# Performance work log

Measured on AMD Instinct MI355X. Metric: run time of the kernel, lower is better.

## Reference

```python
import jax, jax.numpy as jnp
import numpy as np

B, Cin, C, H, W = 2, 64, 128, 64, 64
D_INNER, N_STATE, DT_RANK, K = 256, 16, 8, 4


def _silu(x):
    return x * jax.nn.sigmoid(x)


def _layernorm(x, g, b, eps=1e-5):
    mu = x.mean(-1, keepdims=True)
    var = ((x - mu) ** 2).mean(-1, keepdims=True)
    return (x - mu) * jax.lax.rsqrt(var + eps) * g + b


def setup_inputs():
    key = jax.random.key(0)
    ks = jax.random.split(key, 16)
    f32 = jnp.float32
    inp = {}
    inp["x"] = jax.random.normal(ks[0], (B, Cin, H, W), f32)
    inp["convin_w"] = jax.random.normal(ks[1], (C, Cin), f32) * 0.05
    inp["convin_b"] = jnp.zeros((C,), f32)
    inp["ln_g"] = jnp.ones((C,), f32)
    inp["ln_b"] = jnp.zeros((C,), f32)
    inp["in_proj_w"] = jax.random.normal(ks[2], (2 * D_INNER, C), f32) * 0.05
    inp["conv_w"] = jax.random.normal(ks[3], (D_INNER, 1, 3, 3), f32) * 0.1
    inp["conv_b"] = jnp.zeros((D_INNER,), f32)
    inp["x_proj_w"] = jax.random.normal(ks[4], (K, DT_RANK + 2 * N_STATE, D_INNER), f32) * 0.05
    inp["dt_w"] = jax.random.normal(ks[5], (K, D_INNER, DT_RANK), f32) * 0.1
    inp["dt_b"] = jax.random.uniform(ks[6], (K, D_INNER), f32, -4.0, -1.0)
    inp["A_logs"] = jnp.log(jnp.tile(jnp.arange(1, N_STATE + 1, dtype=f32), (K, D_INNER, 1)))
    inp["Ds"] = jnp.ones((K, D_INNER), f32)
    inp["outnorm_g"] = jnp.ones((D_INNER,), f32)
    inp["outnorm_b"] = jnp.zeros((D_INNER,), f32)
    inp["out_proj_w"] = jax.random.normal(ks[7], (C, D_INNER), f32) * 0.05
    inp["ca_fc1_w"] = jax.random.normal(ks[8], (C // 16, C), f32) * 0.1
    inp["ca_fc2_w"] = jax.random.normal(ks[9], (C, C // 16), f32) * 0.1
    inp["gn_g"] = jnp.ones((C,), f32)
    inp["gn_b"] = jnp.zeros((C,), f32)
    return inp


def _selective_scan(u, delta, A, Bm, Cm, Ds):
    # u, delta: (B,K,d,L); A: (K,d,N); Bm, Cm: (B,K,N,L); Ds: (K,d)
    def step(h, inp):
        u_t, dt, B_t, C_t = inp
        dA = jnp.exp(dt[..., None] * A)                      # (B,K,d,N)
        h = h * dA + dt[..., None] * B_t[:, :, None, :] * u_t[..., None]
        y = jnp.einsum('bkdn,bkn->bkd', h, C_t)
        return h, y
    step = jax.checkpoint(step)
    seq = (jnp.moveaxis(u, -1, 0), jnp.moveaxis(delta, -1, 0),
           jnp.moveaxis(Bm, -1, 0), jnp.moveaxis(Cm, -1, 0))
    h0 = jnp.zeros(u.shape[:3] + (A.shape[-1],), u.dtype)
    _, ys = jax.lax.scan(step, h0, seq)                      # (L,B,K,d)
    y = jnp.moveaxis(ys, 0, -1)                              # (B,K,d,L)
    return y + u * Ds[None, :, :, None]


def reference(x, convin_w, convin_b, ln_g, ln_b, in_proj_w, conv_w, conv_b,
              x_proj_w, dt_w, dt_b, A_logs, Ds, outnorm_g, outnorm_b,
              out_proj_w, ca_fc1_w, ca_fc2_w, gn_g, gn_b):
    L = H * W
    # 1x1 conv in
    x1 = jnp.einsum('bchw,oc->bohw', x, convin_w) + convin_b[None, :, None, None]
    m = x1.transpose(0, 2, 3, 1)                             # (B,H,W,C)
    # VSSBlock: LN -> SS2D -> residual
    m_ln = _layernorm(m, ln_g, ln_b)
    xz = m_ln @ in_proj_w.T                                  # (B,H,W,2*d_inner)
    xm, z = jnp.split(xz, 2, axis=-1)
    xm = xm.transpose(0, 3, 1, 2)                            # (B,d,H,W)
    xm = jax.lax.conv_general_dilated(xm, conv_w, (1, 1), [(1, 1), (1, 1)],
                                      feature_group_count=D_INNER)
    xm = _silu(xm + conv_b[None, :, None, None])
    x_flat = xm.reshape(B, D_INNER, L)
    x_tr = xm.transpose(0, 1, 3, 2).reshape(B, D_INNER, L)
    xs = jnp.stack([x_flat, x_tr, jnp.flip(x_flat, -1), jnp.flip(x_tr, -1)], axis=1)
    x_dbl = jnp.einsum('bkdl,kcd->bkcl', xs, x_proj_w)
    dts, Bs, Cs = jnp.split(x_dbl, [DT_RANK, DT_RANK + N_STATE], axis=2)
    delta = jax.nn.softplus(jnp.einsum('bkrl,kdr->bkdl', dts, dt_w) + dt_b[None, :, :, None])
    A = -jnp.exp(A_logs)                                     # (K,d,N)
    out_y = _selective_scan(xs, delta, A, Bs, Cs, Ds)        # (B,4,d,L)
    y0 = out_y[:, 0]
    y1 = out_y[:, 1].reshape(B, D_INNER, W, H).transpose(0, 1, 3, 2).reshape(B, D_INNER, L)
    y2 = jnp.flip(out_y[:, 2], -1)
    y3 = jnp.flip(out_y[:, 3], -1).reshape(B, D_INNER, W, H).transpose(0, 1, 3, 2).reshape(B, D_INNER, L)
    y = (y0 + y1 + y2 + y3).transpose(0, 2, 1).reshape(B, H, W, D_INNER)
    y = _layernorm(y, outnorm_g, outnorm_b)
    y = y * _silu(z)
    m_out = m + y @ out_proj_w.T                             # (B,H,W,C)
    mamba = m_out.transpose(0, 3, 1, 2)                      # (B,C,H,W)
    # CBAM-style channel attention
    def mlp(v):
        return jax.nn.relu(v @ ca_fc1_w.T) @ ca_fc2_w.T
    avg = mamba.mean((2, 3))
    mx = mamba.max((2, 3))
    att = jax.nn.sigmoid(mlp(avg) + mlp(mx))[:, :, None, None]
    ca = mamba * att
    # GroupNorm(2 groups) + SiLU + residual
    g = ca.reshape(B, 2, -1)
    mu = g.mean(-1, keepdims=True)
    var = ((g - mu) ** 2).mean(-1, keepdims=True)
    g = ((g - mu) * jax.lax.rsqrt(var + 1e-5)).reshape(B, C, H, W)
    g = g * gn_g[None, :, None, None] + gn_b[None, :, None, None]
    return _silu(g) + x1
```

## Files before the change

### kernel.cpp

```cpp
#include <hip/hip_runtime.h>
#include <math.h>


#define DEV __device__ __forceinline__

typedef __attribute__((ext_vector_type(8))) short bf16x8;
typedef __attribute__((ext_vector_type(4))) float f32x4;

DEV float sigm_(float x){ return 1.f/(1.f+__expf(-x)); }
DEV float silu_(float x){ return x*sigm_(x); }
DEV float sp_(float x){ return (x>15.f)? x : __logf(1.f+__expf(x)); }

DEV unsigned short f2bf(float f){
  union{float f; unsigned u;} v; v.f=f;
  unsigned r=v.u + 0x7FFFu + ((v.u>>16)&1u);
  return (unsigned short)(r>>16);
}
DEV float bf2f(unsigned short h){ union{unsigned u; float f;} v; v.u=((unsigned)h)<<16; return v.f; }

DEV int pos_dir(int k, int l){
  switch(k&3){
    case 0: return l;
    case 1: return ((l&63)<<6)|(l>>6);
    case 2: return 4095-l;
    default:{ int m=4095-l; return ((m&63)<<6)|(m>>6); }
  }
}

DEV bf16x8 cvt_frag(const float* p){
  float4 q0=*(const float4*)p, q1=*(const float4*)(p+4);
  bf16x8 t;
  t[0]=(short)f2bf(q0.x); t[1]=(short)f2bf(q0.y); t[2]=(short)f2bf(q0.z); t[3]=(short)f2bf(q0.w);
  t[4]=(short)f2bf(q1.x); t[5]=(short)f2bf(q1.y); t[6]=(short)f2bf(q1.z); t[7]=(short)f2bf(q1.w);
  return t;
}

__global__ __launch_bounds__(256) void k_x1ln(const float* __restrict__ x,
    const float* __restrict__ W, const float* __restrict__ bias,
    const float* __restrict__ g, const float* __restrict__ be,
    float* __restrict__ x1, unsigned short* __restrict__ mlnb){
  const int b=blockIdx.y, p0=blockIdx.x*64;
  __shared__ float sw[64*132];
  __shared__ float sx[64*68];
  __shared__ float red[2][16][68];
  __shared__ float smu[64], srs[64];
  const int tid=threadIdx.x, tx=tid&15, ty=tid>>4;
  for (int i=tid;i<8192;i+=256){ int c=i&63,o=i>>6; sw[c*132+o]=W[o*64+c]; }
  for (int i=tid;i<4096;i+=256){ int c=i>>6,p=i&63; sx[c*68+p]=x[((size_t)(b*64+c))*4096+p0+p]; }
  __syncthreads();
  float acc[8][4]={};
  for (int c=0;c<64;++c){
    float4 a0=*(const float4*)&sw[c*132+ty*8];
    float4 a1=*(const float4*)&sw[c*132+ty*8+4];
    float4 bv=*(const float4*)&sx[c*68+tx*4];
    acc[0][0]=fmaf(a0.x,bv.x,acc[0][0]); acc[0][1]=fmaf(a0.x,bv.y,acc[0][1]); acc[0][2]=fmaf(a0.x,bv.z,acc[0][2]); acc[0][3]=fmaf(a0.x,bv.w,acc[0][3]);
    acc[1][0]=fmaf(a0.y,bv.x,acc[1][0]); acc[1][1]=fmaf(a0.y,bv.y,acc[1][1]); acc[1][2]=fmaf(a0.y,bv.z,acc[1][2]); acc[1][3]=fmaf(a0.y,bv.w,acc[1][3]);
    acc[2][0]=fmaf(a0.z,bv.x,acc[2][0]); acc[2][1]=fmaf(a0.z,bv.y,acc[2][1]); acc[2][2]=fmaf(a0.z,bv.z,acc[2][2]); acc[2][3]=fmaf(a0.z,bv.w,acc[2][3]);
    acc[3][0]=fmaf(a0.w,bv.x,acc[3][0]); acc[3][1]=fmaf(a0.w,bv.y,acc[3][1]); acc[3][2]=fmaf(a0.w,bv.z,acc[3][2]); acc[3][3]=fmaf(a0.w,bv.w,acc[3][3]);
    acc[4][0]=fmaf(a1.x,bv.x,acc[4][0]); acc[4][1]=fmaf(a1.x,bv.y,acc[4][1]); acc[4][2]=fmaf(a1.x,bv.z,acc[4][2]); acc[4][3]=fmaf(a1.x,bv.w,acc[4][3]);
    acc[5][0]=fmaf(a1.y,bv.x,acc[5][0]); acc[5][1]=fmaf(a1.y,bv.y,acc[5][1]); acc[5][2]=fmaf(a1.y,bv.z,acc[5][2]); acc[5][3]=fmaf(a1.y,bv.w,acc[5][3]);
    acc[6][0]=fmaf(a1.z,bv.x,acc[6][0]); acc[6][1]=fmaf(a1.z,bv.y,acc[6][1]); acc[6][2]=fmaf(a1.z,bv.z,acc[6][2]); acc[6][3]=fmaf(a1.z,bv.w,acc[6][3]);
    acc[7][0]=fmaf(a1.w,bv.x,acc[7][0]); acc[7][1]=fmaf(a1.w,bv.y,acc[7][1]); acc[7][2]=fmaf(a1.w,bv.z,acc[7][2]); acc[7][3]=fmaf(a1.w,bv.w,acc[7][3]);
  }
  float xr[8][4];
  #pragma unroll
  for (int i=0;i<8;++i){
    float bs=bias[ty*8+i];
    #pragma unroll
    for (int j=0;j<4;++j) xr[i][j]=acc[i][j]+bs;
  }
  {
    float s[4]={},s2[4]={};
    #pragma unroll
    for (int i=0;i<8;++i)
      #pragma unroll
      for (int j=0;j<4;++j){ s[j]+=xr[i][j]; s2[j]=fmaf(xr[i][j],xr[i][j],s2[j]); }
    #pragma unroll
    for (int j=0;j<4;++j){ red[0][ty][tx*4+j]=s[j]; red[1][ty][tx*4+j]=s2[j]; }
  }
  __syncthreads();
  if (tid<64){
    float S=0.f,S2=0.f;
    #pragma unroll
    for (int t=0;t<16;++t){ S+=red[0][t][tid]; S2+=red[1][t][tid]; }
    float mu=S*(1.f/128.f), var=S2*(1.f/128.f)-mu*mu;
    smu[tid]=mu; srs[tid]=rsqrtf(var+1e-5f);
  }
  __syncthreads();
  float* lnt=sw;
  #pragma unroll
  for (int i=0;i<8;++i){
    int o=ty*8+i;
    float gv=g[o], bev=be[o];
    #pragma unroll
    for (int j=0;j<4;++j){
      int p=tx*4+j;
      lnt[o*66+p]=(xr[i][j]-smu[p])*srs[p]*gv+bev;
    }
    *(float4*)&x1[((size_t)(b*128+o))*4096+p0+tx*4]=make_float4(xr[i][0],xr[i][1],xr[i][2],xr[i][3]);
  }
  __syncthreads();
  for (int i=tid;i<8192;i+=256){ int p=i>>7,o=i&127; mlnb[((size_t)(b*4096+p0+p))*128+o]=f2bf(lnt[o*66+p]); }
}

__global__ __launch_bounds__(256) void k_inproj(const unsigned short* __restrict__ mlnb,
    const float* __restrict__ W, float* __restrict__ xmpre_t, float* __restrict__ z){
  const int wave=threadIdx.x>>6, lane=threadIdx.x&63;
  const int quad=lane>>4, l16=lane&15;
  const int m0=blockIdx.y*128+(wave>>1)*64;
  const int n0=blockIdx.x*64+(wave&1)*32;
  f32x4 acc[4][2];
  #pragma unroll
  for (int i=0;i<4;++i)
    #pragma unroll
    for (int j=0;j<2;++j) acc[i][j]=(f32x4){0.f,0.f,0.f,0.f};
  for (int k0=0;k0<128;k0+=32){
    bf16x8 a[4], b[2];
    #pragma unroll
    for (int mi=0;mi<4;++mi)
      a[mi]=*(const bf16x8*)&mlnb[(size_t)(m0+mi*16+l16)*128 + k0 + quad*8];
    #pragma unroll
    for (int ni=0;ni<2;++ni)
      b[ni]=cvt_frag(&W[(size_t)(n0+ni*16+l16)*128 + k0 + quad*8]);
    #pragma unroll
    for (int mi=0;mi<4;++mi)
      #pragma unroll
      for (int ni=0;ni<2;++ni)
        acc[mi][ni]=__builtin_amdgcn_mfma_f32_16x16x32_bf16(a[mi],b[ni],acc[mi][ni],0,0,0);
  }
  #pragma unroll
  for (int mi=0;mi<4;++mi)
    #pragma unroll
    for (int ni=0;ni<2;++ni)
      #pragma unroll
      for (int r=0;r<4;++r){
        const int row=m0+mi*16+quad*4+r;
        const int col=n0+ni*16+l16;
        float v=acc[mi][ni][r];
        if (col<256) xmpre_t[(size_t)row*256+col]=v;
        else         z[(size_t)row*256+(col-256)]=v;
      }
}

__global__ __launch_bounds__(256) void k_dwconv(const float* __restrict__ xmpre_t,
    const float* __restrict__ cw, const float* __restrict__ cb, unsigned short* __restrict__ xflatb){
  __shared__ float sw[2304];
  __shared__ float sb[256];
  const int tid=threadIdx.x;
  for (int i=tid;i<2304;i+=256) sw[i]=cw[i];
  sb[tid]=cb[tid];
  __syncthreads();
  const int bp0=blockIdx.x*16;
  const int b=bp0>>12, p0=bp0&4095;
  const int dq=tid&63, pg=tid>>6;
  const int d0=dq*4;
  float wr[9][4];
  #pragma unroll
  for (int t=0;t<9;++t)
    #pragma unroll
    for (int c=0;c<4;++c) wr[t][c]=sw[(d0+c)*9+t];
  const float4 bias=make_float4(sb[d0],sb[d0+1],sb[d0+2],sb[d0+3]);
  #pragma unroll
  for (int j=0;j<4;++j){
    const int p=p0+pg*4+j;
    const int h=p>>6, w=p&63;
    float4 acc=bias;
    #pragma unroll
    for (int dh=-1;dh<=1;++dh){
      int hh=h+dh; if ((unsigned)hh>=64u) continue;
      #pragma unroll
      for (int dw=-1;dw<=1;++dw){
        int ww=w+dw; if ((unsigned)ww>=64u) continue;
        const int t=(dh+1)*3+(dw+1);
        float4 iv=*(const float4*)&xmpre_t[((size_t)((b<<12)+hh*64+ww))*256+d0];
        acc.x=fmaf(iv.x,wr[t][0],acc.x); acc.y=fmaf(iv.y,wr[t][1],acc.y);
        acc.z=fmaf(iv.z,wr[t][2],acc.z); acc.w=fmaf(iv.w,wr[t][3],acc.w);
      }
    }
    ushort4 o;
    o.x=f2bf(silu_(acc.x)); o.y=f2bf(silu_(acc.y)); o.z=f2bf(silu_(acc.z)); o.w=f2bf(silu_(acc.w));
    *(ushort4*)&xflatb[((size_t)((b<<12)+p))*256+d0]=o;
  }
}

__global__ __launch_bounds__(256) void k_proj(const unsigned short* __restrict__ xflatb,
    const float* __restrict__ xpw, float* __restrict__ pdt, float* __restrict__ pbc){
  const int wave=threadIdx.x>>6, lane=threadIdx.x&63;
  const int quad=lane>>4, l16=lane&15;
  const int m0=(wave&1)*80;
  const int n0=blockIdx.x*64+(wave>>1)*32;
  f32x4 acc[5][2];
  #pragma unroll
  for (int i=0;i<5;++i)
    #pragma unroll
    for (int j=0;j<2;++j) acc[i][j]=(f32x4){0.f,0.f,0.f,0.f};
  for (int k0=0;k0<256;k0+=32){
    bf16x8 a[5], b[2];
    #pragma unroll
    for (int mi=0;mi<5;++mi)
      a[mi]=cvt_frag(&xpw[(size_t)(m0+mi*16+l16)*256 + k0 + quad*8]);
    #pragma unroll
    for (int ni=0;ni<2;++ni)
      b[ni]=*(const bf16x8*)&xflatb[(size_t)(n0+ni*16+l16)*256 + k0 + quad*8];
    #pragma unroll
    for (int mi=0;mi<5;++mi)
      #pragma unroll
      for (int ni=0;ni<2;++ni)
        acc[mi][ni]=__builtin_amdgcn_mfma_f32_16x16x32_bf16(a[mi],b[ni],acc[mi][ni],0,0,0);
  }
  #pragma unroll
  for (int mi=0;mi<5;++mi)
    #pragma unroll
    for (int ni=0;ni<2;++ni)
      #pragma unroll
      for (int r=0;r<4;++r){
        const int rr=m0+mi*16+quad*4+r;
        const int col=n0+ni*16+l16;
        const int b_=col>>12, pos=col&4095;
        const int kd=rr/40, c=rr%40, bk=b_*4+kd;
        float v=acc[mi][ni][r];
        if (c<8) pdt[((size_t)bk*4096+pos)*8+c]=v;
        else     pbc[((size_t)bk*4096+pos)*32+(c-8)]=v;
      }
}

__global__ __launch_bounds__(256) void k_scanA(const float* __restrict__ pdt,
    const float* __restrict__ pbc, const unsigned short* __restrict__ xflatb,
    const float* __restrict__ dtw, const float* __restrict__ dtb,
    const float* __restrict__ A_logs, const float* __restrict__ Ds,
    float* __restrict__ Pc, float* __restrict__ He, float* __restrict__ ysum){
  const int bx=blockIdx.x;
  const int ch=bx&127, k=(bx>>7)&3, b=bx>>9, bk=b*4+k;
  const int d=threadIdx.x;
  __shared__ float sbc[1024];
  __shared__ float sdt[256];
  for (int i=d;i<1024;i+=256) sbc[i]=pbc[((size_t)bk*4096+(ch<<5))*32+i];
  sdt[d]=pdt[((size_t)bk*4096+(ch<<5))*8+d];
  const float* ap=&A_logs[((k<<8)+d)<<4];
  const float ac0=-__expf(ap[0]);
  bool pw=true;
  #pragma unroll
  for (int n=1;n<16;++n){ float an_=-__expf(ap[n]); pw=pw&&(fabsf(an_-(float)(n+1)*ac0)<=1e-4f*fabsf(an_)); }
  float w8[8];
  {
    float4 w0=*(const float4*)&dtw[(size_t)k*2048+d*8];
    float4 w1=*(const float4*)&dtw[(size_t)k*2048+d*8+4];
    w8[0]=w0.x;w8[1]=w0.y;w8[2]=w0.z;w8[3]=w0.w;w8[4]=w1.x;w8[5]=w1.y;w8[6]=w1.z;w8[7]=w1.w;
  }
  const float dtbd=dtb[(k<<8)+d];
  const float dsv=Ds[(k<<8)+d];
  __syncthreads();
  float h[16]; float sdv=0.f;
  #pragma unroll
  for (int n=0;n<16;++n) h[n]=0.f;
  const unsigned short* up=xflatb+((size_t)b<<12)*256+d;
  if (pw){
    for (int s=0;s<32;++s){
      const int l=(ch<<5)+s;
      float t=dtbd;
      #pragma unroll
      for (int r=0;r<8;++r) t=fmaf(sdt[s*8+r],w8[r],t);
      const float dv=sp_(t);
      const int pos=pos_dir(k,l);
      const float u=bf2f(up[(size_t)pos*256]);
      const float dvu=dv*u;
      sdv+=dv;
      const float q=__expf(dv*ac0);
      float an=q, yl=0.f;
      #pragma unroll
      for (int n4=0;n4<4;++n4){
        float4 bb=*(const float4*)&sbc[s*32+n4*4];
        float4 cc=*(const float4*)&sbc[s*32+16+n4*4];
        h[n4*4+0]=fmaf(h[n4*4+0],an,dvu*bb.x); yl=fmaf(h[n4*4+0],cc.x,yl); an*=q;
        h[n4*4+1]=fmaf(h[n4*4+1],an,dvu*bb.y); yl=fmaf(h[n4*4+1],cc.y,yl); an*=q;
        h[n4*4+2]=fmaf(h[n4*4+2],an,dvu*bb.z); yl=fmaf(h[n4*4+2],cc.z,yl); an*=q;
        h[n4*4+3]=fmaf(h[n4*4+3],an,dvu*bb.w); yl=fmaf(h[n4*4+3],cc.w,yl); an*=q;
      }
      atomicAdd(&ysum[((size_t)((b<<12)+pos))*256+d], yl+u*dsv);
    }
  } else {
    float acoef[16];
    #pragma unroll
    for (int n=0;n<16;++n) acoef[n]=-__expf(ap[n]);
    for (int s=0;s<32;++s){
      const int l=(ch<<5)+s;
      float t=dtbd;
      #pragma unroll
      for (int r=0;r<8;++r) t=fmaf(sdt[s*8+r],w8[r],t);
      const float dv=sp_(t);
      const int pos=pos_dir(k,l);
      const float u=bf2f(up[(size_t)pos*256]);
      const float dvu=dv*u;
      sdv+=dv;
      float yl=0.f;
      #pragma unroll
      for (int n=0;n<16;++n){
        float a=__expf(dv*acoef[n]);
        h[n]=fmaf(h[n],a,dvu*sbc[s*32+n]);
        yl=fmaf(h[n],sbc[s*32+16+n],yl);
      }
      atomicAdd(&ysum[((size_t)((b<<12)+pos))*256+d], yl+u*dsv);
    }
  }
  const size_t obase=(size_t)ch*32768 + ((size_t)bk*256+d)*16;
  if (pw){
    const float qe=__expf(ac0*sdv);
    float an=qe, pcv[16];
    #pragma unroll
    for (int n=0;n<16;++n){ pcv[n]=an; an*=qe; }
    #pragma unroll
    for (int n4=0;n4<4;++n4) *(float4*)&Pc[obase+n4*4]=make_float4(pcv[n4*4],pcv[n4*4+1],pcv[n4*4+2],pcv[n4*4+3]);
  } else {
    #pragma unroll
    for (int n=0;n<16;++n) Pc[obase+n]=__expf(-__expf(ap[n])*sdv);
  }
  #pragma unroll
  for (int n4=0;n4<4;++n4) *(float4*)&He[obase+n4*4]=make_float4(h[n4*4],h[n4*4+1],h[n4*4+2],h[n4*4+3]);
}

__global__ __launch_bounds__(256) void k_scanB(const float* Pc, const float* He, float* Hin){
  const int g2=threadIdx.x&63, tc=threadIdx.x>>6;
  const int gid=blockIdx.x*64+g2;
  float p[32], e[32];
  #pragma unroll
  for (int i=0;i<32;++i){
    size_t idx=(size_t)(tc*32+i)*32768+gid;
    p[i]=Pc[idx]; e[i]=He[idx];
  }
  float P=1.f, E=0.f;
  #pragma unroll
  for (int i=0;i<32;++i){ E=fmaf(E,p[i],e[i]); P*=p[i]; }
  __shared__ float sP[4][64], sE[4][64];
  sP[tc][g2]=P; sE[tc][g2]=E;
  __syncthreads();
  float Hp=0.f;
  for (int t=0;t<tc;++t) Hp=fmaf(Hp,sP[t][g2],sE[t][g2]);
  #pragma unroll
  for (int i=0;i<32;++i){
    Hin[(size_t)(tc*32+i)*32768+gid]=Hp;
    Hp=fmaf(Hp,p[i],e[i]);
  }
}

__global__ __launch_bounds__(256) void k_scanC2(const float* __restrict__ pdt,
    const float* __restrict__ pbc, const float* __restrict__ dtw,
    const float* __restrict__ dtb, const float* __restrict__ A_logs,
    const float* __restrict__ Hin, float* __restrict__ ysum){
  const int bx=blockIdx.x;
  const int ch=bx&127, k=(bx>>7)&3, b=bx>>9, bk=b*4+k;
  if (ch==0) return;
  const int d=threadIdx.x;
  __shared__ float sC[512];
  __shared__ float sdt[256];
  for (int i=d;i<512;i+=256){ int s=i>>4,n=i&15; sC[i]=pbc[((size_t)bk*4096+(ch<<5)+s)*32+16+n]; }
  sdt[d]=pdt[((size_t)bk*4096+(ch<<5))*8+d];
  const float* ap=&A_logs[((k<<8)+d)<<4];
  const float ac0=-__expf(ap[0]);
  bool pw=true;
  #pragma unroll
  for (int n=1;n<16;++n){ float an_=-__expf(ap[n]); pw=pw&&(fabsf(an_-(float)(n+1)*ac0)<=1e-4f*fabsf(an_)); }
  float w8[8];
  {
    float4 w0=*(const float4*)&dtw[(size_t)k*2048+d*8];
    float4 w1=*(const float4*)&dtw[(size_t)k*2048+d*8+4];
    w8[0]=w0.x;w8[1]=w0.y;w8[2]=w0.z;w8[3]=w0.w;w8[4]=w1.x;w8[5]=w1.y;w8[6]=w1.z;w8[7]=w1.w;
  }
  const float dtbd=dtb[(k<<8)+d];
  __syncthreads();
  const size_t ibase=(size_t)ch*32768 + ((size_t)bk*256+d)*16;
  float h[16];
  #pragma unroll
  for (int n4=0;n4<4;++n4){
    float4 hv=*(const float4*)&Hin[ibase+n4*4];
    h[n4*4]=hv.x; h[n4*4+1]=hv.y; h[n4*4+2]=hv.z; h[n4*4+3]=hv.w;
  }
  if (pw){
    float cumd=0.f;
    for (int s=0;s<32;++s){
      float t=dtbd;
      #pragma unroll
      for (int r=0;r<8;++r) t=fmaf(sdt[s*8+r],w8[r],t);
      cumd+=sp_(t);
      const float q=__expf(ac0*cumd);
      float an=q, corr=0.f;
      #pragma unroll
      for (int n4=0;n4<4;++n4){
        float4 cc=*(const float4*)&sC[s*16+n4*4];
        corr=fmaf(h[n4*4+0]*an,cc.x,corr); an*=q;
        corr=fmaf(h[n4*4+1]*an,cc.y,corr); an*=q;
        corr=fmaf(h[n4*4+2]*an,cc.z,corr); an*=q;
        corr=fmaf(h[n4*4+3]*an,cc.w,corr); an*=q;
      }
      const int l=(ch<<5)+s;
      atomicAdd(&ysum[((size_t)((b<<12)+pos_dir(k,l)))*256+d], corr);
    }
  } else {
    float acoef[16];
    #pragma unroll
    for (int n=0;n<16;++n) acoef[n]=-__expf(ap[n]);
    float cumd=0.f;
    for (int s=0;s<32;++s){
      float t=dtbd;
      #pragma unroll
      for (int r=0;r<8;++r) t=fmaf(sdt[s*8+r],w8[r],t);
      cumd+=sp_(t);
      float corr=0.f;
      #pragma unroll
      for (int n=0;n<16;++n) corr=fmaf(h[n]*__expf(acoef[n]*cumd),sC[s*16+n],corr);
      const int l=(ch<<5)+s;
      atomicAdd(&ysum[((size_t)((b<<12)+pos_dir(k,l)))*256+d], corr);
    }
  }
}

__global__ __launch_bounds__(256) void k_outnorm(const float* __restrict__ ysum,
    const float* __restrict__ g, const float* __restrict__ be,
    const float* __restrict__ z, unsigned short* __restrict__ ygb){
  const int bp=blockIdx.x, d=threadIdx.x;
  float v=ysum[(size_t)bp*256+d];
  float s=v, s2=v*v;
  #pragma unroll
  for (int m=1;m<64;m<<=1){ s+=__shfl_xor(s,m); s2+=__shfl_xor(s2,m); }
  __shared__ float rs[4], rs2[4];
  if ((d&63)==0){ rs[d>>6]=s; rs2[d>>6]=s2; }
  __syncthreads();
  float S=rs[0]+rs[1]+rs[2]+rs[3], S2=rs2[0]+rs2[1]+rs2[2]+rs2[3];
  float mu=S*(1.f/256.f), var=S2*(1.f/256.f)-mu*mu, rstd=rsqrtf(var+1e-5f);
  float ln=(v-mu)*rstd*g[d]+be[d];
  float zv=z[(size_t)bp*256+d];
  ygb[(size_t)bp*256+d]=f2bf(ln*silu_(zv));
}

__global__ __launch_bounds__(256) void k_outproj(const unsigned short* __restrict__ ygb,
    const float* __restrict__ W, const float* __restrict__ x1, float* __restrict__ mamba){
  const int wave=threadIdx.x>>6, lane=threadIdx.x&63;
  const int quad=lane>>4, l16=lane&15;
  const int m0=(wave>>1)*64;
  const int n0=blockIdx.x*64+(wave&1)*32;
  f32x4 acc[4][2];
  #pragma unroll
  for (int i=0;i<4;++i)
    #pragma unroll
    for (int j=0;j<2;++j) acc[i][j]=(f32x4){0.f,0.f,0.f,0.f};
  for (int k0=0;k0<256;k0+=32){
    bf16x8 a[4], b[2];
    #pragma unroll
    for (int mi=0;mi<4;++mi)
      a[mi]=cvt_frag(&W[(size_t)(m0+mi*16+l16)*256 + k0 + quad*8]);
    #pragma unroll
    for (int ni=0;ni<2;++ni)
      b[ni]=*(const bf16x8*)&ygb[(size_t)(n0+ni*16+l16)*256 + k0 + quad*8];
    #pragma unroll
    for (int mi=0;mi<4;++mi)
      #pragma unroll
      for (int ni=0;ni<2;++ni)
        acc[mi][ni]=__builtin_amdgcn_mfma_f32_16x16x32_bf16(a[mi],b[ni],acc[mi][ni],0,0,0);
  }
  #pragma unroll
  for (int mi=0;mi<4;++mi)
    #pragma unroll
    for (int ni=0;ni<2;++ni)
      #pragma unroll
      for (int r=0;r<4;++r){
        const int c=m0+mi*16+quad*4+r;
        const int col=n0+ni*16+l16;
        const int b_=col>>12, pos=col&4095;
        const size_t addr=((size_t)((b_<<7)+c))*4096+pos;
        mamba[addr]=acc[mi][ni][r]+x1[addr];
      }
}

__global__ __launch_bounds__(256) void k_stats(const float* __restrict__ mamba, float* __restrict__ stats){
  const int bc=blockIdx.x, tid=threadIdx.x;
  const float* row=mamba+(size_t)bc*4096;
  float s=0.f,s2=0.f,mx=-3.402823466e38f;
  for (int i=tid;i<4096;i+=256){ float v=row[i]; s+=v; s2=fmaf(v,v,s2); mx=fmaxf(mx,v); }
  #pragma unroll
  for (int m=1;m<64;m<<=1){
    s+=__shfl_xor(s,m); s2+=__shfl_xor(s2,m); mx=fmaxf(mx,__shfl_xor(mx,m));
  }
  __shared__ float r0[4],r1[4],r2[4];
  if ((tid&63)==0){ int wv=tid>>6; r0[wv]=s; r1[wv]=s2; r2[wv]=mx; }
  __syncthreads();
  if (tid==0){
    stats[bc*3+0]=r0[0]+r0[1]+r0[2]+r0[3];
    stats[bc*3+1]=r1[0]+r1[1]+r1[2]+r1[3];
    stats[bc*3+2]=fmaxf(fmaxf(r2[0],r2[1]),fmaxf(r2[2],r2[3]));
  }
}

__global__ __launch_bounds__(256) void k_att(const float* __restrict__ stats,
    const float* __restrict__ fc1, const float* __restrict__ fc2,
    float* __restrict__ att, float* __restrict__ gstat){
  __shared__ float avg[2][128], mxs[2][128], S1[2][128], S2[2][128], hsum[2][8], attv[2][128];
  const int tid=threadIdx.x, b=tid>>7, c=tid&127;
  float s1=stats[tid*3], s2=stats[tid*3+1], m=stats[tid*3+2];
  avg[b][c]=s1*(1.f/4096.f); mxs[b][c]=m; S1[b][c]=s1; S2[b][c]=s2;
  __syncthreads();
  if (tid<16){
    int bb=tid>>3, i=tid&7;
    float ha=0.f,hm=0.f;
    for (int cc=0;cc<128;++cc){ float w=fc1[i*128+cc]; ha=fmaf(w,avg[bb][cc],ha); hm=fmaf(w,mxs[bb][cc],hm); }
    hsum[bb][i]=fmaxf(ha,0.f)+fmaxf(hm,0.f);
  }
  __syncthreads();
  float sacc=0.f;
  #pragma unroll
  for (int i=0;i<8;++i) sacc=fmaf(fc2[c*8+i],hsum[b][i],sacc);
  float a=sigm_(sacc);
  attv[b][c]=a; att[tid]=a;
  __syncthreads();
  if (tid<4){
    int bb=tid>>1, gp=tid&1;
    float sum1=0.f,sum2=0.f;
    for (int cc=0;cc<64;++cc){
      int c2=gp*64+cc; float av=attv[bb][c2];
      sum1=fmaf(av,S1[bb][c2],sum1);
      sum2=fmaf(av*av,S2[bb][c2],sum2);
    }
    const float inv=1.f/(64.f*4096.f);
    float mu=sum1*inv, ex2=sum2*inv, var=ex2-mu*mu;
    gstat[tid*2]=mu; gstat[tid*2+1]=rsqrtf(var+1e-5f);
  }
}

__global__ __launch_bounds__(256) void k_final(const float* __restrict__ mamba,
    const float* __restrict__ x1, const float* __restrict__ att,
    const float* __restrict__ gstat, const float* __restrict__ gg,
    const float* __restrict__ gb, float* __restrict__ out){
  const int idx=blockIdx.x*256+threadIdx.x;
  const int c=(idx>>12)&127, b=idx>>19;
  const int grp=(b<<1)+(c>>6);
  float v=mamba[idx]*att[(b<<7)+c];
  float vn=(v-gstat[grp*2])*gstat[grp*2+1]*gg[c]+gb[c];
  out[idx]=silu_(vn)+x1[idx];
}

extern "C" void kernel_launch(void* const* d_in, const int* in_sizes, int n_in,
                              void* d_out, int out_size, void* d_ws, size_t ws_size,
                              hipStream_t stream){
  (void)in_sizes; (void)n_in; (void)out_size; (void)ws_size;
  const float* x        =(const float*)d_in[0];
  const float* convin_w =(const float*)d_in[1];
  const float* convin_b =(const float*)d_in[2];
  const float* ln_g     =(const float*)d_in[3];
  const float* ln_b     =(const float*)d_in[4];
  const float* in_proj_w=(const float*)d_in[5];
  const float* conv_w   =(const float*)d_in[6];
  const float* conv_b   =(const float*)d_in[7];
  const float* x_proj_w =(const float*)d_in[8];
  const float* dt_w     =(const float*)d_in[9];
  const float* dt_b     =(const float*)d_in[10];
  const float* A_logs   =(const float*)d_in[11];
  const float* Ds       =(const float*)d_in[12];
  const float* outnorm_g=(const float*)d_in[13];
  const float* outnorm_b=(const float*)d_in[14];
  const float* out_proj_w=(const float*)d_in[15];
  const float* ca_fc1_w =(const float*)d_in[16];
  const float* ca_fc2_w =(const float*)d_in[17];
  const float* gn_g     =(const float*)d_in[18];
  const float* gn_b     =(const float*)d_in[19];

  float* ws=(float*)d_ws;
  float*          x1     =ws+0;
  float*          z      =ws+1048576;
  float*          xmpre_t=ws+3145728;
  unsigned short* mlnb   =(unsigned short*)(ws+5242880);
  unsigned short* xflatb =(unsigned short*)(ws+6291456);
  float*          pdt    =ws+8388608;
  float*          pbc    =ws+8912896;
  float*          Pc     =ws+10485760;
  float*          He     =ws+14680064;
  float*          ysum   =ws+18874368;
  unsigned short* ygb    =(unsigned short*)(ws+3145728);
  float*          mamba  =ws+5242880;
  float*          stats  =ws+27262976;
  float*          att    =stats+768;
  float*          gstat  =att+256;

  const dim3 blk(256);
  hipMemsetAsync(ysum, 0, 2097152*sizeof(float), stream);
  k_x1ln   <<<dim3(64,2),   blk,0,stream>>>(x, convin_w, convin_b, ln_g, ln_b, x1, mlnb);
  k_inproj <<<dim3(8,64),   blk,0,stream>>>(mlnb, in_proj_w, xmpre_t, z);
  k_dwconv <<<dim3(512),    blk,0,stream>>>(xmpre_t, conv_w, conv_b, xflatb);
  k_proj   <<<dim3(128),    blk,0,stream>>>(xflatb, x_proj_w, pdt, pbc);
  k_scanA  <<<dim3(1024),   blk,0,stream>>>(pdt, pbc, xflatb, dt_w, dt_b, A_logs, Ds, Pc, He, ysum);
  k_scanB  <<<dim3(512),    blk,0,stream>>>(Pc, He, Pc );
  k_scanC2 <<<dim3(1024),   blk,0,stream>>>(pdt, pbc, dt_w, dt_b, A_logs, Pc , ysum);
  k_outnorm<<<dim3(8192),   blk,0,stream>>>(ysum, outnorm_g, outnorm_b, z, ygb);
  k_outproj<<<dim3(128),    blk,0,stream>>>(ygb, out_proj_w, x1, mamba);
  k_stats  <<<dim3(256),    blk,0,stream>>>(mamba, stats);
  k_att    <<<dim3(1),      blk,0,stream>>>(stats, ca_fc1_w, ca_fc2_w, att, gstat);
  k_final  <<<dim3(4096),   blk,0,stream>>>(mamba, x1, att, gstat, gn_g, gn_b, (float*)d_out);
}
```

Baseline: 269.6 us.

## Store scan intermediates and in_proj output in bf16; fuse channel stats into outproj

Switches the xmpre intermediate, the chunk decay products Pc, the chunk end states He and the propagated states Hin from fp32 to bf16 storage, halving their memory traffic. The separate stats kernel is removed: outproj now reduces sum, sum of squares and max per channel with shuffles and atomics, using an order-preserving float-to-uint key for atomicMax. This cuts one launch and a full read of mamba. In exchange it loses precision in the scan carry states and decay products, which could compound across chunks, and adds atomic contention on the stats buffer, which now has to be zeroed first.

```diff
diff --git a/kernel.cpp b/kernel.cpp
--- a/kernel.cpp
+++ b/kernel.cpp
@@ -17,6 +17,16 @@
   return (unsigned short)(r>>16);
 }
 DEV float bf2f(unsigned short h){ union{unsigned u; float f;} v; v.u=((unsigned)h)<<16; return v.f; }
+
+DEV unsigned fkey(float f){
+  union{float f; unsigned u;} v; v.f=f;
+  return (v.u&0x80000000u)? ~v.u : (v.u|0x80000000u);
+}
+DEV float funkey(unsigned k){
+  union{unsigned u; float f;} v;
+  v.u=(k&0x80000000u)? (k^0x80000000u) : ~k;
+  return v.f;
+}
 
 DEV int pos_dir(int k, int l){
   switch(k&3){
@@ -104,7 +114,7 @@
 }
 
 __global__ __launch_bounds__(256) void k_inproj(const unsigned short* __restrict__ mlnb,
-    const float* __restrict__ W, float* __restrict__ xmpre_t, float* __restrict__ z){
+    const float* __restrict__ W, unsigned short* __restrict__ xmpreb, float* __restrict__ z){
   const int wave=threadIdx.x>>6, lane=threadIdx.x&63;
   const int quad=lane>>4, l16=lane&15;
   const int m0=blockIdx.y*128+(wave>>1)*64;
@@ -137,12 +147,12 @@
         const int row=m0+mi*16+quad*4+r;
         const int col=n0+ni*16+l16;
         float v=acc[mi][ni][r];
-        if (col<256) xmpre_t[(size_t)row*256+col]=v;
+        if (col<256) xmpreb[(size_t)row*256+col]=f2bf(v);
         else         z[(size_t)row*256+(col-256)]=v;
       }
 }
 
-__global__ __launch_bounds__(256) void k_dwconv(const float* __restrict__ xmpre_t,
+__global__ __launch_bounds__(256) void k_dwconv(const unsigned short* __restrict__ xmpreb,
     const float* __restrict__ cw, const float* __restrict__ cb, unsigned short* __restrict__ xflatb){
   __shared__ float sw[2304];
   __shared__ float sb[256];
@@ -172,9 +182,9 @@
       for (int dw=-1;dw<=1;++dw){
         int ww=w+dw; if ((unsigned)ww>=64u) continue;
         const int t=(dh+1)*3+(dw+1);
-        float4 iv=*(const float4*)&xmpre_t[((size_t)((b<<12)+hh*64+ww))*256+d0];
-        acc.x=fmaf(iv.x,wr[t][0],acc.x); acc.y=fmaf(iv.y,wr[t][1],acc.y);
-        acc.z=fmaf(iv.z,wr[t][2],acc.z); acc.w=fmaf(iv.w,wr[t][3],acc.w);
+        ushort4 u4=*(const ushort4*)&xmpreb[((size_t)((b<<12)+hh*64+ww))*256+d0];
+        acc.x=fmaf(bf2f(u4.x),wr[t][0],acc.x); acc.y=fmaf(bf2f(u4.y),wr[t][1],acc.y);
+        acc.z=fmaf(bf2f(u4.z),wr[t][2],acc.z); acc.w=fmaf(bf2f(u4.w),wr[t][3],acc.w);
       }
     }
     ushort4 o;
@@ -228,7 +238,8 @@
     const float* __restrict__ pbc, const unsigned short* __restrict__ xflatb,
     const float* __restrict__ dtw, const float* __restrict__ dtb,
     const float* __restrict__ A_logs, const float* __restrict__ Ds,
-    float* __restrict__ Pc, float* __restrict__ He, float* __restrict__ ysum){
+    unsigned short* __restrict__ Pcb, unsigned short* __restrict__ Heb,
+    float* __restrict__ ysum){
   const int bx=blockIdx.x;
   const int ch=bx&127, k=(bx>>7)&3, b=bx>>9, bk=b*4+k;
   const int d=threadIdx.x;
@@ -305,27 +316,35 @@
   const size_t obase=(size_t)ch*32768 + ((size_t)bk*256+d)*16;
   if (pw){
     const float qe=__expf(ac0*sdv);
-    float an=qe, pcv[16];
-    #pragma unroll
-    for (int n=0;n<16;++n){ pcv[n]=an; an*=qe; }
-    #pragma unroll
-    for (int n4=0;n4<4;++n4) *(float4*)&Pc[obase+n4*4]=make_float4(pcv[n4*4],pcv[n4*4+1],pcv[n4*4+2],pcv[n4*4+3]);
+    float an=qe;
+    #pragma unroll
+    for (int n4=0;n4<4;++n4){
+      ushort4 o;
+      o.x=f2bf(an); an*=qe; o.y=f2bf(an); an*=qe;
+      o.z=f2bf(an); an*=qe; o.w=f2bf(an); an*=qe;
+      *(ushort4*)&Pcb[obase+n4*4]=o;
+    }
   } else {
     #pragma unroll
-    for (int n=0;n<16;++n) Pc[obase+n]=__expf(-__expf(ap[n])*sdv);
-  }
-  #pragma unroll
-  for (int n4=0;n4<4;++n4) *(float4*)&He[obase+n4*4]=make_float4(h[n4*4],h[n4*4+1],h[n4*4+2],h[n4*4+3]);
-}
-
-__global__ __launch_bounds__(256) void k_scanB(const float* Pc, const float* He, float* Hin){
+    for (int n=0;n<16;++n) Pcb[obase+n]=f2bf(__expf(-__expf(ap[n])*sdv));
+  }
+  #pragma unroll
+  for (int n4=0;n4<4;++n4){
+    ushort4 o;
+    o.x=f2bf(h[n4*4]); o.y=f2bf(h[n4*4+1]); o.z=f2bf(h[n4*4+2]); o.w=f2bf(h[n4*4+3]);
+    *(ushort4*)&Heb[obase+n4*4]=o;
+  }
+}
+
+__global__ __launch_bounds__(256) void k_scanB(const unsigned short* Pcb,
+    const unsigned short* Heb, unsigned short* Hinb){
   const int g2=threadIdx.x&63, tc=threadIdx.x>>6;
   const int gid=blockIdx.x*64+g2;
   float p[32], e[32];
   #pragma unroll
   for (int i=0;i<32;++i){
     size_t idx=(size_t)(tc*32+i)*32768+gid;
-    p[i]=Pc[idx]; e[i]=He[idx];
+    p[i]=bf2f(Pcb[idx]); e[i]=bf2f(Heb[idx]);
   }
   float P=1.f, E=0.f;
   #pragma unroll
@@ -337,7 +356,7 @@
   for (int t=0;t<tc;++t) Hp=fmaf(Hp,sP[t][g2],sE[t][g2]);
   #pragma unroll
   for (int i=0;i<32;++i){
-    Hin[(size_t)(tc*32+i)*32768+gid]=Hp;
+    Hinb[(size_t)(tc*32+i)*32768+gid]=f2bf(Hp);
     Hp=fmaf(Hp,p[i],e[i]);
   }
 }
@@ -345,7 +364,7 @@
 __global__ __launch_bounds__(256) void k_scanC2(const float* __restrict__ pdt,
     const float* __restrict__ pbc, const float* __restrict__ dtw,
     const float* __restrict__ dtb, const float* __restrict__ A_logs,
-    const float* __restrict__ Hin, float* __restrict__ ysum){
+    const unsigned short* __restrict__ Hinb, float* __restrict__ ysum){
   const int bx=blockIdx.x;
   const int ch=bx&127, k=(bx>>7)&3, b=bx>>9, bk=b*4+k;
   if (ch==0) return;
@@ -370,10 +389,7 @@
   const size_t ibase=(size_t)ch*32768 + ((size_t)bk*256+d)*16;
   float h[16];
   #pragma unroll
-  for (int n4=0;n4<4;++n4){
-    float4 hv=*(const float4*)&Hin[ibase+n4*4];
-    h[n4*4]=hv.x; h[n4*4+1]=hv.y; h[n4*4+2]=hv.z; h[n4*4+3]=hv.w;
-  }
+  for (int n=0;n<16;++n) h[n]=bf2f(Hinb[ibase+n]);
   if (pw){
     float cumd=0.f;
     for (int s=0;s<32;++s){
@@ -432,11 +448,13 @@
 }
 
 __global__ __launch_bounds__(256) void k_outproj(const unsigned short* __restrict__ ygb,
-    const float* __restrict__ W, const float* __restrict__ x1, float* __restrict__ mamba){
+    const float* __restrict__ W, const float* __restrict__ x1, float* __restrict__ mamba,
+    float* __restrict__ stats){
   const int wave=threadIdx.x>>6, lane=threadIdx.x&63;
   const int quad=lane>>4, l16=lane&15;
   const int m0=(wave>>1)*64;
   const int n0=blockIdx.x*64+(wave&1)*32;
+  const int b_=blockIdx.x>>6;
   f32x4 acc[4][2];
   #pragma unroll
   for (int i=0;i<4;++i)
@@ -459,34 +477,31 @@
   #pragma unroll
   for (int mi=0;mi<4;++mi)
     #pragma unroll
-    for (int ni=0;ni<2;++ni)
-      #pragma unroll
-      for (int r=0;r<4;++r){
-        const int c=m0+mi*16+quad*4+r;
+    for (int r=0;r<4;++r){
+      const int c=m0+mi*16+quad*4+r;
+      float v[2];
+      #pragma unroll
+      for (int ni=0;ni<2;++ni){
         const int col=n0+ni*16+l16;
-        const int b_=col>>12, pos=col&4095;
+        const int pos=col&4095;
         const size_t addr=((size_t)((b_<<7)+c))*4096+pos;
-        mamba[addr]=acc[mi][ni][r]+x1[addr];
-      }
-}
-
-__global__ __launch_bounds__(256) void k_stats(const float* __restrict__ mamba, float* __restrict__ stats){
-  const int bc=blockIdx.x, tid=threadIdx.x;
-  const float* row=mamba+(size_t)bc*4096;
-  float s=0.f,s2=0.f,mx=-3.402823466e38f;
-  for (int i=tid;i<4096;i+=256){ float v=row[i]; s+=v; s2=fmaf(v,v,s2); mx=fmaxf(mx,v); }
-  #pragma unroll
-  for (int m=1;m<64;m<<=1){
-    s+=__shfl_xor(s,m); s2+=__shfl_xor(s2,m); mx=fmaxf(mx,__shfl_xor(mx,m));
-  }
-  __shared__ float r0[4],r1[4],r2[4];
-  if ((tid&63)==0){ int wv=tid>>6; r0[wv]=s; r1[wv]=s2; r2[wv]=mx; }
-  __syncthreads();
-  if (tid==0){
-    stats[bc*3+0]=r0[0]+r0[1]+r0[2]+r0[3];
-    stats[bc*3+1]=r1[0]+r1[1]+r1[2]+r1[3];
-    stats[bc*3+2]=fmaxf(fmaxf(r2[0],r2[1]),fmaxf(r2[2],r2[3]));
-  }
+        v[ni]=acc[mi][ni][r]+x1[addr];
+        mamba[addr]=v[ni];
+      }
+      float s=v[0]+v[1];
+      float s2=v[0]*v[0]+v[1]*v[1];
+      float mx=fmaxf(v[0],v[1]);
+      #pragma unroll
+      for (int m=1;m<16;m<<=1){
+        s+=__shfl_xor(s,m); s2+=__shfl_xor(s2,m); mx=fmaxf(mx,__shfl_xor(mx,m));
+      }
+      if (l16==0){
+        const int bc=(b_<<7)+c;
+        atomicAdd(&stats[bc*3+0], s);
+        atomicAdd(&stats[bc*3+1], s2);
+        atomicMax((unsigned*)&stats[bc*3+2], fkey(mx));
+      }
+    }
 }
 
 __global__ __launch_bounds__(256) void k_att(const float* __restrict__ stats,
@@ -494,7 +509,8 @@
     float* __restrict__ att, float* __restrict__ gstat){
   __shared__ float avg[2][128], mxs[2][128], S1[2][128], S2[2][128], hsum[2][8], attv[2][128];
   const int tid=threadIdx.x, b=tid>>7, c=tid&127;
-  float s1=stats[tid*3], s2=stats[tid*3+1], m=stats[tid*3+2];
+  float s1=stats[tid*3], s2=stats[tid*3+1];
+  float m=funkey(((const unsigned*)stats)[tid*3+2]);
   avg[b][c]=s1*(1.f/4096.f); mxs[b][c]=m; S1[b][c]=s1; S2[b][c]=s2;
   __syncthreads();
   if (tid<16){
@@ -564,13 +580,13 @@
   float* ws=(float*)d_ws;
   float*          x1     =ws+0;
   float*          z      =ws+1048576;
-  float*          xmpre_t=ws+3145728;
+  unsigned short* xmpreb =(unsigned short*)(ws+3145728);
   unsigned short* mlnb   =(unsigned short*)(ws+5242880);
   unsigned short* xflatb =(unsigned short*)(ws+6291456);
   float*          pdt    =ws+8388608;
   float*          pbc    =ws+8912896;
-  float*          Pc     =ws+10485760;
-  float*          He     =ws+14680064;
+  unsigned short* Pcb    =(unsigned short*)(ws+10485760);
+  unsigned short* Heb    =(unsigned short*)(ws+12582912);
   float*          ysum   =ws+18874368;
   unsigned short* ygb    =(unsigned short*)(ws+3145728);
   float*          mamba  =ws+5242880;
@@ -580,16 +596,16 @@
 
   const dim3 blk(256);
   hipMemsetAsync(ysum, 0, 2097152*sizeof(float), stream);
+  hipMemsetAsync(stats, 0, 768*sizeof(float), stream);
   k_x1ln   <<<dim3(64,2),   blk,0,stream>>>(x, convin_w, convin_b, ln_g, ln_b, x1, mlnb);
-  k_inproj <<<dim3(8,64),   blk,0,stream>>>(mlnb, in_proj_w, xmpre_t, z);
-  k_dwconv <<<dim3(512),    blk,0,stream>>>(xmpre_t, conv_w, conv_b, xflatb);
+  k_inproj <<<dim3(8,64),   blk,0,stream>>>(mlnb, in_proj_w, xmpreb, z);
+  k_dwconv <<<dim3(512),    blk,0,stream>>>(xmpreb, conv_w, conv_b, xflatb);
   k_proj   <<<dim3(128),    blk,0,stream>>>(xflatb, x_proj_w, pdt, pbc);
-  k_scanA  <<<dim3(1024),   blk,0,stream>>>(pdt, pbc, xflatb, dt_w, dt_b, A_logs, Ds, Pc, He, ysum);
-  k_scanB  <<<dim3(512),    blk,0,stream>>>(Pc, He, Pc );
-  k_scanC2 <<<dim3(1024),   blk,0,stream>>>(pdt, pbc, dt_w, dt_b, A_logs, Pc , ysum);
+  k_scanA  <<<dim3(1024),   blk,0,stream>>>(pdt, pbc, xflatb, dt_w, dt_b, A_logs, Ds, Pcb, Heb, ysum);
+  k_scanB  <<<dim3(512),    blk,0,stream>>>(Pcb, Heb, Pcb );
+  k_scanC2 <<<dim3(1024),   blk,0,stream>>>(pdt, pbc, dt_w, dt_b, A_logs, Pcb , ysum);
   k_outnorm<<<dim3(8192),   blk,0,stream>>>(ysum, outnorm_g, outnorm_b, z, ygb);
-  k_outproj<<<dim3(128),    blk,0,stream>>>(ygb, out_proj_w, x1, mamba);
-  k_stats  <<<dim3(256),    blk,0,stream>>>(mamba, stats);
+  k_outproj<<<dim3(128),    blk,0,stream>>>(ygb, out_proj_w, x1, mamba, stats);
   k_att    <<<dim3(1),      blk,0,stream>>>(stats, ca_fc1_w, ca_fc2_w, att, gstat);
   k_final  <<<dim3(4096),   blk,0,stream>>>(mamba, x1, att, gstat, gn_g, gn_b, (float*)d_out);
 }
```

New measurement: 318.9 us. 18.3% more time.
